# Kernel tuning notes

Measured on AMD Instinct MI355X. Metric: run time of the kernel, lower is better.

Reference implementation:

```python
import jax, jax.numpy as jnp
import numpy as np

B, L, D = 2, 2048, 2048
H, KVH, HD, FD = 8, 1, 256, 64   # heads, kv heads, head_dim, feature_dim
CHUNK = 64


def setup_inputs() -> dict:
    key = jax.random.key(0)
    ks = jax.random.split(key, 8)
    hidden_states = jax.random.normal(ks[0], (B, L, D), dtype=jnp.float32)
    # Gemma-style RoPE tables over half the head dim
    half = HD // 2
    inv_freq = 1.0 / (10000.0 ** (jnp.arange(half, dtype=jnp.float32) / half))
    ang = jnp.arange(L, dtype=jnp.float32)[:, None] * inv_freq[None, :]  # [L, half]
    freqs_cos, freqs_sin = jnp.cos(ang), jnp.sin(ang)
    mask = jnp.ones((1, 1, L, L), dtype=bool)  # unused in linear path
    s = 0.02
    Wq = jax.random.normal(ks[1], (D, H * HD), dtype=jnp.float32) * s
    Wk = jax.random.normal(ks[2], (D, KVH * HD), dtype=jnp.float32) * s
    Wv = jax.random.normal(ks[3], (D, KVH * HD), dtype=jnp.float32) * s
    Wo = jax.random.normal(ks[4], (H * HD, D), dtype=jnp.float32) * s
    fmq = jax.random.normal(ks[5], (H, HD, FD), dtype=jnp.float32) * s
    fmk = jax.random.normal(ks[6], (H, HD, FD), dtype=jnp.float32) * s
    return dict(hidden_states=hidden_states, freqs_cos=freqs_cos, freqs_sin=freqs_sin,
                mask=mask, Wq=Wq, Wk=Wk, Wv=Wv, Wo=Wo, fmq=fmq, fmk=fmk)


def _rope(x, cos, sin):
    # x: [B, L, h, HD]; Gemma complex RoPE: first half = real, second half = imag
    half = x.shape[-1] // 2
    x1, x2 = x[..., :half], x[..., half:]
    c = cos[None, :, None, :]
    s = sin[None, :, None, :]
    return jnp.concatenate([x1 * c - x2 * s, x1 * s + x2 * c], axis=-1)


def _hedgehog(x, W):
    # x: [B, H, L, HD], W: [H, HD, FD] -> softmax over cat([xW, -xW]) -> [B,H,L,2*FD]
    p = jnp.einsum('bhld,hdf->bhlf', x, W)
    return jax.nn.softmax(jnp.concatenate([p, -p], axis=-1), axis=-1)


def _chunk_linear_attn(q, k, v, chunk=CHUNK):
    # q,k: [B,H,L,F]; v: [B,H,L,HD]; chunked causal linear attention
    b, h, l, f = q.shape
    dv = v.shape[-1]
    n = l // chunk
    q = q.reshape(b, h, n, chunk, f) * (f ** -0.5)
    k = k.reshape(b, h, n, chunk, f)
    v = v.reshape(b, h, n, chunk, dv)
    kv = jnp.einsum('bhncf,bhncd->bhnfd', k, v)            # per-chunk KV
    kv = jnp.cumsum(kv, axis=2)
    kv = jnp.concatenate([jnp.zeros_like(kv[:, :, :1]), kv[:, :, :-1]], axis=2)  # exclusive prefix
    inter = jnp.einsum('bhncf,bhnfd->bhncd', q, kv)        # cross-chunk term
    s = jnp.einsum('bhnif,bhnjf->bhnij', q, k)             # intra-chunk scores
    tri = jnp.tril(jnp.ones((chunk, chunk), dtype=bool))
    s = jnp.where(tri, s, 0.0)
    intra = jnp.einsum('bhnij,bhnjd->bhnid', s, v)
    return (inter + intra).reshape(b, h, l, dv)


def reference(hidden_states, freqs_cos, freqs_sin, mask, Wq, Wk, Wv, Wo, fmq, fmk):
    b, l, _ = hidden_states.shape
    q = (hidden_states @ Wq).reshape(b, l, H, HD)
    k = (hidden_states @ Wk).reshape(b, l, KVH, HD)
    v = (hidden_states @ Wv).reshape(b, l, KVH, HD)
    q = _rope(q, freqs_cos, freqs_sin)
    k = _rope(k, freqs_cos, freqs_sin)
    # repeat_interleave kv heads to num_heads (MQA expansion)
    rep = H // KVH
    k = jnp.repeat(k, rep, axis=2)
    v = jnp.repeat(v, rep, axis=2)
    q = jnp.transpose(q, (0, 2, 1, 3))  # [B,H,L,HD]
    k = jnp.transpose(k, (0, 2, 1, 3))
    v = jnp.transpose(v, (0, 2, 1, 3))
    q = _hedgehog(q, fmq)
    k = _hedgehog(k, fmk)
    o = _chunk_linear_attn(q, k, v)                         # [B,H,L,HD]
    o = jnp.transpose(o, (0, 2, 1, 3)).reshape(b, l, H * HD)
    return o @ Wo
```

## Files before the change

kernel.cpp:

```cpp
#include <hip/hip_runtime.h>

#define B_ 2
#define L_ 2048
#define D_ 2048
#define H_ 8
#define HD_ 256
#define FD_ 64
#define F_ 128
#define NC_ 32
#define M_ (B_*L_)
#define SCALE_Q 0.08838834764831845f

typedef unsigned short u16;
typedef __attribute__((ext_vector_type(8))) short bf16x8;
typedef __attribute__((ext_vector_type(8))) unsigned short u16x8;
typedef __attribute__((ext_vector_type(16))) float f32x16;
typedef __attribute__((ext_vector_type(4))) unsigned int u32x4;

#define FMA4(a_, s_, v_) { (a_).x += (s_)*(v_).x; (a_).y += (s_)*(v_).y; \
                           (a_).z += (s_)*(v_).z; (a_).w += (s_)*(v_).w; }


__device__ __forceinline__ u16 bf16_rne(float x) {
  unsigned u = __float_as_uint(x);
  return (u16)((u + 0x7fffu + ((u >> 16) & 1u)) >> 16);
}
__device__ __forceinline__ void bf16_split(float x, u16& h, u16& l) {
  unsigned u = __float_as_uint(x);
  unsigned hb = (u + 0x7fffu + ((u >> 16) & 1u)) >> 16;
  h = (u16)hb;
  float hf = __uint_as_float(hb << 16);
  l = bf16_rne(x - hf);
}

__device__ __forceinline__ void gl_lds16(const u16* g, u16* l) {
  __builtin_amdgcn_global_load_lds(
      (const __attribute__((address_space(1))) unsigned int*)g,
      (__attribute__((address_space(3))) unsigned int*)l, 16, 0, 0);
}

__device__ __forceinline__ size_t kvb_off(int d, int f) {
  return (size_t)(((d >> 7) & 1) * 16384 + ((f >> 5) & 3) * 4096 +
                  ((d >> 6) & 1) * 2048 + ((f >> 4) & 1) * 1024 +
                  ((d >> 5) & 1) * 512 + ((f >> 3) & 1) * 256 +
                  (d & 31) * 8 + (f & 7));
}

__device__ __forceinline__ void wtrans_body(const float* __restrict__ W, int Nsrc,
                                            int n0, u16* __restrict__ dst,
                                            int P, int kt) {
  int t = threadIdx.x;
  int nn = t & 127, kh = t >> 7;
  const float* src = W + (size_t)(kt * 32 + kh * 16) * Nsrc + n0 + nn;
  u16x8 u0, u1;
  #pragma unroll
  for (int kk = 0; kk < 8; ++kk) u0[kk] = bf16_rne(src[(size_t)kk * Nsrc]);
  #pragma unroll
  for (int kk = 0; kk < 8; ++kk) u1[kk] = bf16_rne(src[(size_t)(kk + 8) * Nsrc]);
  size_t base = ((size_t)P * 64 + kt) * 4096 + (size_t)((nn >> 6) & 1) * 2048
              + (size_t)kh * 1024 + (size_t)((nn >> 5) & 1) * 512
              + (size_t)(nn & 31) * 8;
  *(u16x8*)(dst + base) = u0;
  *(u16x8*)(dst + base + 256) = u1;
}

__global__ __launch_bounds__(256)
void prep_kernel(const float* __restrict__ hs,
                 const float* __restrict__ Wq, const float* __restrict__ Wk,
                 const float* __restrict__ Wv,
                 u16* __restrict__ hsHt, u16* __restrict__ hsLt,
                 u16* __restrict__ WTh) {
  int bid = blockIdx.x;
  if (bid < 4096) {
    int gid = bid * 256 + threadIdx.x;
    int r = gid >> 8, u = gid & 255;
    const float* src = hs + (size_t)r * 2048 + u * 8;
    float4 v0 = *(const float4*)src, v1 = *(const float4*)(src + 4);
    float vals[8] = {v0.x, v0.y, v0.z, v0.w, v1.x, v1.y, v1.z, v1.w};
    u16x8 hv, lv;
    #pragma unroll
    for (int j = 0; j < 8; ++j) { u16 hh, ll; bf16_split(vals[j], hh, ll); hv[j] = hh; lv[j] = ll; }
    size_t off = ((size_t)(r >> 6) * 64 + (u >> 2)) * 2048
               + (size_t)((u >> 1) & 1) * 1024 + (size_t)((r >> 5) & 1) * 512
               + (size_t)(u & 1) * 256 + (size_t)(r & 31) * 8;
    *(u16x8*)(hsHt + off) = hv;
    *(u16x8*)(hsLt + off) = lv;
  } else {
    int idx = bid - 4096;
    int P = idx >> 6, kt = idx & 63;
    const float* W; int Nsrc, n0;
    if (P < 16)      { W = Wq; Nsrc = 2048; n0 = P * 128; }
    else if (P < 18) { W = Wk; Nsrc = 256;  n0 = (P - 16) * 128; }
    else             { W = Wv; Nsrc = 256;  n0 = (P - 18) * 128; }
    wtrans_body(W, Nsrc, n0, WTh, P, kt);
  }
}

__global__ __launch_bounds__(256)
void prep_o(const float* __restrict__ o, u16* __restrict__ oHt,
            u16* __restrict__ oLt) {
  int gid = blockIdx.x * 256 + threadIdx.x;
  int r = gid >> 8, u = gid & 255;
  const float* src = o + (size_t)r * 2048 + u * 8;
  float4 v0 = *(const float4*)src, v1 = *(const float4*)(src + 4);
  float vals[8] = {v0.x, v0.y, v0.z, v0.w, v1.x, v1.y, v1.z, v1.w};
  u16x8 hv, lv;
  #pragma unroll
  for (int j = 0; j < 8; ++j) { u16 hh, ll; bf16_split(vals[j], hh, ll); hv[j] = hh; lv[j] = ll; }
  size_t off = ((size_t)(r >> 6) * 64 + (u >> 2)) * 2048
             + (size_t)((u >> 1) & 1) * 1024 + (size_t)((r >> 5) & 1) * 512
             + (size_t)(u & 1) * 256 + (size_t)(r & 31) * 8;
  *(u16x8*)(oHt + off) = hv;
  *(u16x8*)(oLt + off) = lv;
}

__global__ __launch_bounds__(256)
void wtrans_wo(const float* __restrict__ Wo, u16* __restrict__ WoTh) {
  wtrans_body(Wo, 2048, blockIdx.x * 128, WoTh, blockIdx.x, blockIdx.y);
}

__device__ __forceinline__ void mfma_body(
    const u16* __restrict__ AtH, const u16* __restrict__ AtL,
    const u16* __restrict__ Bt, float* __restrict__ C, int cstride,
    int bm, int bn) {
  __shared__ __align__(16) u16 AsH[2048];
  __shared__ __align__(16) u16 AsL[2048];
  __shared__ __align__(16) u16 Bs[4096];
  const int t = threadIdx.x, lane = t & 63, wv = t >> 6;
  const u16* aSrc = (wv ? AtL : AtH) + (size_t)bm * 131072 + lane * 8;
  const u16* bSrc = Bt + (size_t)bn * 262144 + wv * 2048 + lane * 8;
  u16* aDst = wv ? AsL : AsH;
  u16* bDst = Bs + wv * 2048;

  f32x16 acc[2][2];
  #pragma unroll
  for (int a = 0; a < 2; ++a)
    #pragma unroll
    for (int b2 = 0; b2 < 2; ++b2)
      #pragma unroll
      for (int r = 0; r < 16; ++r) acc[a][b2][r] = 0.f;

  for (int kt = 0; kt < 64; ++kt) {
    const u16* ak = aSrc + (size_t)kt * 2048;
    const u16* bk = bSrc + (size_t)kt * 4096;
    __syncthreads();
    #pragma unroll
    for (int c = 0; c < 4; ++c) {
      gl_lds16(ak + c * 512, aDst + c * 512);
      gl_lds16(bk + c * 512, bDst + c * 512);
    }
    __syncthreads();

    #pragma unroll
    for (int ks = 0; ks < 2; ++ks) {
      const u16* ph = AsH + ks * 1024 + lane * 8;
      const u16* pl = AsL + ks * 1024 + lane * 8;
      const u16* pb = Bs + wv * 2048 + ks * 1024 + lane * 8;
      bf16x8 a0 = *(const bf16x8*)ph;
      bf16x8 a1 = *(const bf16x8*)(ph + 512);
      bf16x8 b0 = *(const bf16x8*)pb;
      bf16x8 b1 = *(const bf16x8*)(pb + 512);
      acc[0][0] = __builtin_amdgcn_mfma_f32_32x32x16_bf16(a0, b0, acc[0][0], 0, 0, 0);
      acc[0][1] = __builtin_amdgcn_mfma_f32_32x32x16_bf16(a0, b1, acc[0][1], 0, 0, 0);
      acc[1][0] = __builtin_amdgcn_mfma_f32_32x32x16_bf16(a1, b0, acc[1][0], 0, 0, 0);
      acc[1][1] = __builtin_amdgcn_mfma_f32_32x32x16_bf16(a1, b1, acc[1][1], 0, 0, 0);
      bf16x8 l0 = *(const bf16x8*)pl;
      bf16x8 l1 = *(const bf16x8*)(pl + 512);
      acc[0][0] = __builtin_amdgcn_mfma_f32_32x32x16_bf16(l0, b0, acc[0][0], 0, 0, 0);
      acc[0][1] = __builtin_amdgcn_mfma_f32_32x32x16_bf16(l0, b1, acc[0][1], 0, 0, 0);
      acc[1][0] = __builtin_amdgcn_mfma_f32_32x32x16_bf16(l1, b0, acc[1][0], 0, 0, 0);
      acc[1][1] = __builtin_amdgcn_mfma_f32_32x32x16_bf16(l1, b1, acc[1][1], 0, 0, 0);
    }
  }

  const int fr = lane & 31, g = lane >> 5;
  float* Cp = C + (size_t)(bm * 64) * cstride + wv * 64;
  #pragma unroll
  for (int mt = 0; mt < 2; ++mt)
    #pragma unroll
    for (int nt = 0; nt < 2; ++nt) {
      #pragma unroll
      for (int r = 0; r < 16; ++r) {
        int row = mt * 32 + (r & 3) + 8 * (r >> 2) + 4 * g;
        Cp[(size_t)row * cstride + nt * 32 + fr] = acc[mt][nt][r];
      }
    }
}

#define SUB_ 20480

__device__ __forceinline__ void mfma_big_body(
    const u16* __restrict__ AtH, const u16* __restrict__ AtL,
    const u16* __restrict__ Bt, float* __restrict__ C, int cstride,
    int bm, int bn) {
  __shared__ __align__(16) u16 lds[3 * SUB_];
  const int t = threadIdx.x, lane = t & 63, wv = t >> 6;
  const int wm = wv >> 1, wn = wv & 1;

  const u16* gs[5];
  unsigned lo[5], gst[5];
  #pragma unroll
  for (int j = 0; j < 5; ++j) {
    int line = wv * 5 + j;
    if (line < 16) {
      gs[j] = AtH + ((size_t)(4 * bm + (line >> 2)) * 64) * 2048
                  + (size_t)(line & 3) * 512 + lane * 8;
      lo[j] = line * 512; gst[j] = 2048;
    } else if (line < 32) {
      int l2 = line - 16;
      gs[j] = AtL + ((size_t)(4 * bm + (l2 >> 2)) * 64) * 2048
                  + (size_t)(l2 & 3) * 512 + lane * 8;
      lo[j] = 8192 + l2 * 512; gst[j] = 2048;
    } else {
      int l3 = line - 32;
      gs[j] = Bt + (size_t)bn * 262144 + (size_t)l3 * 512 + lane * 8;
      lo[j] = 16384 + l3 * 512; gst[j] = 4096;
    }
  }

  f32x16 acc[2][2];
  #pragma unroll
  for (int a = 0; a < 2; ++a)
    #pragma unroll
    for (int b2 = 0; b2 < 2; ++b2)
      #pragma unroll
      for (int r = 0; r < 16; ++r) acc[a][b2][r] = 0.f;

  auto stage = [&](int kt_, int boff_) {
    #pragma unroll
    for (int j = 0; j < 5; ++j)
      gl_lds16(gs[j] + (size_t)kt_ * gst[j], lds + boff_ + lo[j]);
  };

  stage(0, 0);
  stage(1, SUB_);
  asm volatile("s_waitcnt vmcnt(5)" ::: "memory");
  __builtin_amdgcn_s_barrier();
  __builtin_amdgcn_sched_barrier(0);

  int cb = 0;
  for (int kt = 0; kt < 64; ++kt) {
    int sb = cb + 2 * SUB_; if (sb >= 3 * SUB_) sb -= 3 * SUB_;
    if (kt < 62) stage(kt + 2, sb);
    const u16* base = lds + cb;
    #pragma unroll
    for (int ks = 0; ks < 2; ++ks) {
      const u16* ph = base + wm * 2048 + ks * 1024 + lane * 8;
      const u16* pb = base + 16384 + wn * 2048 + ks * 1024 + lane * 8;
      bf16x8 a0 = *(const bf16x8*)ph;
      bf16x8 a1 = *(const bf16x8*)(ph + 512);
      bf16x8 l0 = *(const bf16x8*)(ph + 8192);
      bf16x8 l1 = *(const bf16x8*)(ph + 8704);
      bf16x8 b0 = *(const bf16x8*)pb;
      bf16x8 b1 = *(const bf16x8*)(pb + 512);
      __builtin_amdgcn_s_setprio(1);
      acc[0][0] = __builtin_amdgcn_mfma_f32_32x32x16_bf16(a0, b0, acc[0][0], 0, 0, 0);
      acc[0][1] = __builtin_amdgcn_mfma_f32_32x32x16_bf16(a0, b1, acc[0][1], 0, 0, 0);
      acc[1][0] = __builtin_amdgcn_mfma_f32_32x32x16_bf16(a1, b0, acc[1][0], 0, 0, 0);
      acc[1][1] = __builtin_amdgcn_mfma_f32_32x32x16_bf16(a1, b1, acc[1][1], 0, 0, 0);
      acc[0][0] = __builtin_amdgcn_mfma_f32_32x32x16_bf16(l0, b0, acc[0][0], 0, 0, 0);
      acc[0][1] = __builtin_amdgcn_mfma_f32_32x32x16_bf16(l0, b1, acc[0][1], 0, 0, 0);
      acc[1][0] = __builtin_amdgcn_mfma_f32_32x32x16_bf16(l1, b0, acc[1][0], 0, 0, 0);
      acc[1][1] = __builtin_amdgcn_mfma_f32_32x32x16_bf16(l1, b1, acc[1][1], 0, 0, 0);
      __builtin_amdgcn_s_setprio(0);
    }
    asm volatile("s_waitcnt lgkmcnt(0)" ::: "memory");
    if (kt < 62) asm volatile("s_waitcnt vmcnt(5)" ::: "memory");
    else         asm volatile("s_waitcnt vmcnt(0)" ::: "memory");
    __builtin_amdgcn_s_barrier();
    __builtin_amdgcn_sched_barrier(0);
    cb += SUB_; if (cb == 3 * SUB_) cb = 0;
  }

  const int fr = lane & 31, g = lane >> 5;
  float* Cp = C + (size_t)(bm * 256 + wm * 64) * cstride + wn * 64;
  #pragma unroll
  for (int mt = 0; mt < 2; ++mt)
    #pragma unroll
    for (int nt = 0; nt < 2; ++nt) {
      #pragma unroll
      for (int r = 0; r < 16; ++r) {
        int row = mt * 32 + (r & 3) + 8 * (r >> 2) + 4 * g;
        Cp[(size_t)row * cstride + nt * 32 + fr] = acc[mt][nt][r];
      }
    }
}

__global__ __launch_bounds__(512, 2)
void mfma_q(const u16* __restrict__ hsHt, const u16* __restrict__ hsLt,
            const u16* __restrict__ WTh, float* __restrict__ q) {
  mfma_big_body(hsHt, hsLt, WTh, q + blockIdx.x * 128, 2048,
                blockIdx.y, blockIdx.x);
}

__global__ __launch_bounds__(128, 4)
void mfma_kv(const u16* __restrict__ hsHt, const u16* __restrict__ hsLt,
             const u16* __restrict__ WTh,
             float* __restrict__ k, float* __restrict__ v) {
  int bn = blockIdx.x;
  float* Cb; int co;
  if (bn < 2) { Cb = k; co = bn * 128; }
  else        { Cb = v; co = (bn - 2) * 128; }
  mfma_body(hsHt, hsLt, WTh, Cb + co, 256, blockIdx.y, 16 + bn);
}

__global__ __launch_bounds__(512, 2)
void mfma_wo(const u16* __restrict__ oHt, const u16* __restrict__ oLt,
             const u16* __restrict__ WoTh, float* __restrict__ out) {
  mfma_big_body(oHt, oLt, WoTh, out + blockIdx.x * 128, 2048,
                blockIdx.y, blockIdx.x);
}

__device__ __forceinline__ float wave_max64(float v) {
  #pragma unroll
  for (int off = 32; off > 0; off >>= 1) v = fmaxf(v, __shfl_xor(v, off, 64));
  return v;
}
__device__ __forceinline__ float wave_sum64(float v) {
  #pragma unroll
  for (int off = 32; off > 0; off >>= 1) v += __shfl_xor(v, off, 64);
  return v;
}

__global__ __launch_bounds__(256)
void hedgehog_kernel(const float* __restrict__ q, const float* __restrict__ kx,
                     const float* __restrict__ fmq, const float* __restrict__ fmk,
                     const float* __restrict__ cosb, const float* __restrict__ sinb,
                     float* __restrict__ qf, float* __restrict__ kf) {
  __shared__ __align__(16) float rows[4][4][256];
  int bid = blockIdx.x;
  const float* x; const float* fm; float* out; int nh_in, gb;
  if (bid < 2048) { x = q;  fm = fmq; out = qf; nh_in = 8; gb = bid * 4; }
  else            { x = kx; fm = fmk; out = kf; nh_in = 1; gb = (bid - 2048) * 4; }
  int wave = threadIdx.x >> 6, lane = threadIdx.x & 63;
  int g = gb + wave;
  int l4 = g & (L_/4 - 1);
  int bh = g / (L_/4);
  int h = bh & 7, b = bh >> 3;
  int l0 = l4 * 4;
  size_t rstride = (nh_in == 1) ? (size_t)HD_ : (size_t)H_ * HD_;
  const float* xrow = (nh_in == 1)
      ? x + (size_t)(b * L_ + l0) * HD_
      : x + ((size_t)(b * L_ + l0) * H_ + h) * HD_;
  int dd = (lane & 31) * 4;
  #pragma unroll
  for (int r = 0; r < 4; ++r) {
    float4 v = *(const float4*)(xrow + r * rstride + lane * 4);
    float4 u;
    u.x = __shfl_xor(v.x, 32, 64); u.y = __shfl_xor(v.y, 32, 64);
    u.z = __shfl_xor(v.z, 32, 64); u.w = __shfl_xor(v.w, 32, 64);
    int l = l0 + r;
    float4 c = *(const float4*)(cosb + (size_t)l * 128 + dd);
    float4 s = *(const float4*)(sinb + (size_t)l * 128 + dd);
    float4 ro;
    if (lane < 32) {
      ro.x = v.x * c.x - u.x * s.x; ro.y = v.y * c.y - u.y * s.y;
      ro.z = v.z * c.z - u.z * s.z; ro.w = v.w * c.w - u.w * s.w;
    } else {
      ro.x = u.x * s.x + v.x * c.x; ro.y = u.y * s.y + v.y * c.y;
      ro.z = u.z * s.z + v.z * c.z; ro.w = u.w * s.w + v.w * c.w;
    }
    *(float4*)&rows[wave][r][lane * 4] = ro;
  }
  __syncthreads();

  const float* fmh = fm + (size_t)h * HD_ * FD_;
  float p0 = 0.f, p1 = 0.f, p2 = 0.f, p3 = 0.f;
  for (int d2 = 0; d2 < HD_; d2 += 4) {
    float w0 = fmh[(d2 + 0) * FD_ + lane];
    float w1 = fmh[(d2 + 1) * FD_ + lane];
    float w2 = fmh[(d2 + 2) * FD_ + lane];
    float w3 = fmh[(d2 + 3) * FD_ + lane];
    float4 r0 = *(const float4*)&rows[wave][0][d2];
    float4 r1 = *(const float4*)&rows[wave][1][d2];
    float4 r2 = *(const float4*)&rows[wave][2][d2];
    float4 r3 = *(const float4*)&rows[wave][3][d2];
    p0 += r0.x * w0 + r0.y * w1 + r0.z * w2 + r0.w * w3;
    p1 += r1.x * w0 + r1.y * w1 + r1.z * w2 + r1.w * w3;
    p2 += r2.x * w0 + r2.y * w1 + r2.z * w2 + r2.w * w3;
    p3 += r3.x * w0 + r3.y * w1 + r3.z * w2 + r3.w * w3;
  }
  float p[4] = {p0, p1, p2, p3};
  #pragma unroll
  for (int r = 0; r < 4; ++r) {
    float m = wave_max64(fabsf(p[r]));
    float e1 = __expf(p[r] - m);
    float e2 = __expf(-p[r] - m);
    float z = wave_sum64(e1 + e2);
    float inv = 1.0f / z;
    size_t base = ((size_t)bh * L_ + l0 + r) * F_;
    out[base + lane]      = e1 * inv;
    out[base + 64 + lane] = e2 * inv;
  }
}

__global__ __launch_bounds__(256)
void chunk_kv_kernel(const float* __restrict__ kf, const float* __restrict__ v,
                     u16* __restrict__ kvbH, u16* __restrict__ kvbL) {
  __shared__ __align__(16) float kfs[64][128];
  int n = blockIdx.x & (NC_ - 1), bh = blockIdx.x >> 5;
  int b = bh >> 3;
  const float* kfp = kf + ((size_t)bh * L_ + (size_t)n * 64) * F_;
  int t = threadIdx.x;
  #pragma unroll
  for (int it = 0; it < 8; ++it) {
    int flat = t * 4 + it * 1024;
    *(float4*)&kfs[flat >> 7][flat & 127] = *(const float4*)(kfp + flat);
  }
  __syncthreads();
  int dg = t & 63;
  int fg = t >> 6;
  const float* vp = v + (size_t)(b * L_ + n * 64) * HD_ + dg * 4;
  size_t cb = (size_t)blockIdx.x * 32768;
  #pragma unroll
  for (int pass = 0; pass < 4; ++pass) {
    int f0 = fg * 8 + pass * 32;
    float4 acc[8];
    #pragma unroll
    for (int i = 0; i < 8; ++i) acc[i] = make_float4(0.f, 0.f, 0.f, 0.f);
    for (int j = 0; j < 64; ++j) {
      float4 vv = *(const float4*)(vp + (size_t)j * HD_);
      float4 ka = *(const float4*)&kfs[j][f0];
      float4 kb = *(const float4*)&kfs[j][f0 + 4];
      FMA4(acc[0], ka.x, vv); FMA4(acc[1], ka.y, vv);
      FMA4(acc[2], ka.z, vv); FMA4(acc[3], ka.w, vv);
      FMA4(acc[4], kb.x, vv); FMA4(acc[5], kb.y, vv);
      FMA4(acc[6], kb.z, vv); FMA4(acc[7], kb.w, vv);
    }
    #pragma unroll
    for (int c = 0; c < 4; ++c) {
      u16x8 hv, lv;
      #pragma unroll
      for (int ff = 0; ff < 8; ++ff) {
        float xs = (c == 0) ? acc[ff].x : (c == 1) ? acc[ff].y
                 : (c == 2) ? acc[ff].z : acc[ff].w;
        u16 hh, ll; bf16_split(xs, hh, ll); hv[ff] = hh; lv[ff] = ll;
      }
      int d = dg * 4 + c;
      size_t off = cb + kvb_off(d, f0);
      *(u16x8*)(kvbH + off) = hv;
      *(u16x8*)(kvbL + off) = lv;
    }
  }
}

__global__ __launch_bounds__(256)
void chunk_scan_kernel(u16* __restrict__ kvbH, u16* __restrict__ kvbL) {
  int bh = blockIdx.x >> 4, g = blockIdx.x & 15;
  int d = threadIdx.x;
  size_t off = kvb_off(d, g * 8);
  float run[8] = {0.f, 0.f, 0.f, 0.f, 0.f, 0.f, 0.f, 0.f};
  for (int n = 0; n < NC_; ++n) {
    size_t a = ((size_t)(bh * 32 + n)) * 32768 + off;
    u16x8 hv = *(u16x8*)(kvbH + a);
    u16x8 lv = *(u16x8*)(kvbL + a);
    u16x8 oh, ol;
    #pragma unroll
    for (int c = 0; c < 8; ++c) {
      float val = __uint_as_float((unsigned)hv[c] << 16)
                + __uint_as_float((unsigned)lv[c] << 16);
      u16 hh, ll; bf16_split(run[c], hh, ll); oh[c] = hh; ol[c] = ll;
      run[c] += val;
    }
    *(u16x8*)(kvbH + a) = oh;
    *(u16x8*)(kvbL + a) = ol;
  }
}

#define MFB(a_, b_, c_) (c_) = __builtin_amdgcn_mfma_f32_32x32x16_bf16((a_), (b_), (c_), 0, 0, 0)

__global__ __launch_bounds__(256, 2)
void chunk_attn_kernel(const float* __restrict__ qf, const float* __restrict__ kf,
                       const float* __restrict__ v,
                       const u16* __restrict__ kvbH, const u16* __restrict__ kvbL,
                       float* __restrict__ o) {
  __shared__ __align__(16) u16 lds[32768];
  const int n = blockIdx.x & (NC_ - 1), bh = blockIdx.x >> 5;
  const int h = bh & 7, b = bh >> 3;
  const int t = threadIdx.x;
  const int w = t >> 6, i31 = t & 31, G = (t >> 5) & 1;
  const int l8 = (t & 63) * 8;

  {
    const float* qp = qf + ((size_t)bh * L_ + (size_t)n * 64) * F_;
    const float* kp = kf + ((size_t)bh * L_ + (size_t)n * 64) * F_;
    int o8 = t & 15, ib = t >> 4;
    #pragma unroll
    for (int iter = 0; iter < 4; ++iter) {
      int i = ib + iter * 16;
      int it = i >> 5, ks = o8 >> 1;
      int sub = (it * 8 + ks) * 512 + (o8 & 1) * 256 + (i & 31) * 8;
      {
        const float* src = qp + (size_t)i * 128 + o8 * 8;
        float4 a = *(const float4*)src, c = *(const float4*)(src + 4);
        float vals[8] = {a.x, a.y, a.z, a.w, c.x, c.y, c.z, c.w};
        u16x8 hv, lv;
        #pragma unroll
        for (int j = 0; j < 8; ++j) {
          u16 hh, ll; bf16_split(vals[j] * SCALE_Q, hh, ll);
          hv[j] = hh; lv[j] = ll;
        }
        *(u16x8*)(lds + sub) = hv;
        *(u16x8*)(lds + 8192 + sub) = lv;
      }
      {
        const float* src = kp + (size_t)i * 128 + o8 * 8;
        float4 a = *(const float4*)src, c = *(const float4*)(src + 4);
        float vals[8] = {a.x, a.y, a.z, a.w, c.x, c.y, c.z, c.w};
        u16x8 hv, lv;
        #pragma unroll
        for (int j = 0; j < 8; ++j) {
          u16 hh, ll; bf16_split(vals[j], hh, ll);
          hv[j] = hh; lv[j] = ll;
        }
        *(u16x8*)(lds + 16384 + sub) = hv;
        *(u16x8*)(lds + 24576 + sub) = lv;
      }
    }
  }
  __syncthreads();

  const u16* Lq  = lds;
  const u16* Lql = lds + 8192;
  const u16* Lk  = lds + 16384;
  const u16* Lkl = lds + 24576;

  f32x16 st[2][2];
  #pragma unroll
  for (int a = 0; a < 2; ++a)
    #pragma unroll
    for (int c = 0; c < 2; ++c)
      #pragma unroll
      for (int r = 0; r < 16; ++r) st[a][c][r] = 0.f;

  #pragma unroll
  for (int ks = 0; ks < 8; ++ks) {
    bf16x8 kh0 = *(const bf16x8*)(Lk  + ks * 512 + l8);
    bf16x8 kh1 = *(const bf16x8*)(Lk  + (8 + ks) * 512 + l8);
    bf16x8 kl0 = *(const bf16x8*)(Lkl + ks * 512 + l8);
    bf16x8 kl1 = *(const bf16x8*)(Lkl + (8 + ks) * 512 + l8);
    bf16x8 qh0 = *(const bf16x8*)(Lq  + ks * 512 + l8);
    bf16x8 qh1 = *(const bf16x8*)(Lq  + (8 + ks) * 512 + l8);
    bf16x8 ql0 = *(const bf16x8*)(Lql + ks * 512 + l8);
    bf16x8 ql1 = *(const bf16x8*)(Lql + (8 + ks) * 512 + l8);
    MFB(kh0, qh0, st[0][0]); MFB(kh0, ql0, st[0][0]); MFB(kl0, qh0, st[0][0]);
    MFB(kh0, qh1, st[0][1]); MFB(kh0, ql1, st[0][1]); MFB(kl0, qh1, st[0][1]);
    MFB(kh1, qh0, st[1][0]); MFB(kh1, ql0, st[1][0]); MFB(kl1, qh0, st[1][0]);
    MFB(kh1, qh1, st[1][1]); MFB(kh1, ql1, st[1][1]); MFB(kl1, qh1, st[1][1]);
  }

  bf16x8 sfH[2][4], sfL[2][4];
  #pragma unroll
  for (int mt = 0; mt < 2; ++mt) {
    int iv = mt * 32 + i31;
    #pragma unroll
    for (int ksj = 0; ksj < 4; ++ksj) {
      const int jt = ksj >> 1, kb = ksj & 1;
      unsigned ph[4], pl[4];
      #pragma unroll
      for (int half = 0; half < 2; ++half) {
        u16 hh[4], ll[4];
        #pragma unroll
        for (int c = 0; c < 4; ++c) {
          int r = 8 * kb + 4 * half + c;
          int jv = jt * 32 + (r & 3) + 8 * (r >> 2) + 4 * G;
          float mv = (jv <= iv) ? st[jt][mt][r] : 0.f;
          u16 h_, l_; bf16_split(mv, h_, l_);
          hh[c] = h_; ll[c] = l_;
        }
        ph[half * 2 + 0] = (unsigned)hh[0] | ((unsigned)hh[1] << 16);
        ph[half * 2 + 1] = (unsigned)hh[2] | ((unsigned)hh[3] << 16);
        pl[half * 2 + 0] = (unsigned)ll[0] | ((unsigned)ll[1] << 16);
        pl[half * 2 + 1] = (unsigned)ll[2] | ((unsigned)ll[3] << 16);
      }
      unsigned rH1 = (unsigned)__shfl_xor((int)(G ? ph[0] : ph[2]), 32, 64);
      unsigned rH2 = (unsigned)__shfl_xor((int)(G ? ph[1] : ph[3]), 32, 64);
      unsigned rL1 = (unsigned)__shfl_xor((int)(G ? pl[0] : pl[2]), 32, 64);
      unsigned rL2 = (unsigned)__shfl_xor((int)(G ? pl[1] : pl[3]), 32, 64);
      u32x4 wH, wL;
      wH[0] = G ? rH1 : ph[0]; wH[1] = G ? rH2 : ph[1];
      wH[2] = G ? ph[2] : rH1; wH[3] = G ? ph[3] : rH2;
      wL[0] = G ? rL1 : pl[0]; wL[1] = G ? rL2 : pl[1];
      wL[2] = G ? pl[2] : rL1; wL[3] = G ? pl[3] : rL2;
      sfH[mt][ksj] = __builtin_bit_cast(bf16x8, wH);
      sfL[mt][ksj] = __builtin_bit_cast(bf16x8, wL);
    }
  }

  f32x16 acc[2][2];
  #pragma unroll
  for (int a = 0; a < 2; ++a)
    #pragma unroll
    for (int c = 0; c < 2; ++c)
      #pragma unroll
      for (int r = 0; r < 16; ++r) acc[a][c][r] = 0.f;

  {
    const float* vp = v + (size_t)(b * L_ + n * 64) * HD_;
    #pragma unroll
    for (int nt = 0; nt < 2; ++nt) {
      #pragma unroll
      for (int ksj = 0; ksj < 4; ++ksj) {
        const float* vsrc = vp + (size_t)(ksj * 16 + G * 8) * HD_
                          + w * 64 + nt * 32 + i31;
        u16x8 vh, vl;
        #pragma unroll
        for (int c = 0; c < 8; ++c) {
          u16 hh, ll; bf16_split(vsrc[(size_t)c * HD_], hh, ll);
          vh[c] = hh; vl[c] = ll;
        }
        bf16x8 vH = __builtin_bit_cast(bf16x8, vh);
        bf16x8 vL = __builtin_bit_cast(bf16x8, vl);
        MFB(sfH[0][ksj], vH, acc[0][nt]); MFB(sfL[0][ksj], vH, acc[0][nt]);
        MFB(sfH[0][ksj], vL, acc[0][nt]);
        MFB(sfH[1][ksj], vH, acc[1][nt]); MFB(sfL[1][ksj], vH, acc[1][nt]);
        MFB(sfH[1][ksj], vL, acc[1][nt]);
      }
    }
  }

  {
    size_t cb = (size_t)blockIdx.x * 32768;
    #pragma unroll
    for (int ks = 0; ks < 8; ++ks) {
      bf16x8 qa_h0 = *(const bf16x8*)(Lq  + ks * 512 + l8);
      bf16x8 qa_h1 = *(const bf16x8*)(Lq  + (8 + ks) * 512 + l8);
      bf16x8 qa_l0 = *(const bf16x8*)(Lql + ks * 512 + l8);
      bf16x8 qa_l1 = *(const bf16x8*)(Lql + (8 + ks) * 512 + l8);
      #pragma unroll
      for (int nt = 0; nt < 2; ++nt) {
        size_t base = cb + kvb_off(w * 64 + nt * 32, ks * 16) + l8;
        bf16x8 kvH = *(const bf16x8*)((const short*)(kvbH + base));
        bf16x8 kvL = *(const bf16x8*)((const short*)(kvbL + base));
        MFB(qa_h0, kvH, acc[0][nt]); MFB(qa_l0, kvH, acc[0][nt]);
        MFB(qa_h0, kvL, acc[0][nt]);
        MFB(qa_h1, kvH, acc[1][nt]); MFB(qa_l1, kvH, acc[1][nt]);
        MFB(qa_h1, kvL, acc[1][nt]);
      }
    }
  }

  float* op = o + ((size_t)(b * L_ + n * 64)) * 2048 + h * 256 + w * 64;
  #pragma unroll
  for (int mt = 0; mt < 2; ++mt)
    #pragma unroll
    for (int nt = 0; nt < 2; ++nt)
      #pragma unroll
      for (int r = 0; r < 16; ++r) {
        int row = mt * 32 + (r & 3) + 8 * (r >> 2) + 4 * G;
        op[(size_t)row * 2048 + nt * 32 + i31] = acc[mt][nt][r];
      }
}

extern "C" void kernel_launch(void* const* d_in, const int* in_sizes, int n_in,
                              void* d_out, int out_size, void* d_ws, size_t ws_size,
                              hipStream_t stream) {
  const float* hs   = (const float*)d_in[0];
  const float* fcos = (const float*)d_in[1];
  const float* fsin = (const float*)d_in[2];
  const float* Wq  = (const float*)d_in[4];
  const float* Wk  = (const float*)d_in[5];
  const float* Wv  = (const float*)d_in[6];
  const float* Wo  = (const float*)d_in[7];
  const float* fmq = (const float*)d_in[8];
  const float* fmk = (const float*)d_in[9];
  float* out = (float*)d_out;

  float* ws = (float*)d_ws;
  float* q  = ws;
  float* k  = q  + (size_t)M_ * 2048;
  float* v  = k  + (size_t)M_ * 256;
  float* qf = v  + (size_t)M_ * 256;
  float* kf = qf + (size_t)B_ * H_ * L_ * F_;
  float* kvr = kf + (size_t)B_ * H_ * L_ * F_;

  u16* hsHt = (u16*)kvr;
  u16* hsLt = hsHt + (size_t)M_ * 2048;
  u16* WTh  = hsLt + (size_t)M_ * 2048;
  u16* kvbH = (u16*)kvr;
  u16* kvbL = kvbH + (size_t)512 * 32768;
  u16* WoTh = (u16*)kvr;
  float* o  = q;
  u16* oHt  = (u16*)qf;
  u16* oLt  = (u16*)kf;

  prep_kernel<<<4096 + 1280, 256, 0, stream>>>(hs, Wq, Wk, Wv, hsHt, hsLt, WTh);
  mfma_q<<<dim3(16, 16), 512, 0, stream>>>(hsHt, hsLt, WTh, q);
  mfma_kv<<<dim3(4, 64), 128, 0, stream>>>(hsHt, hsLt, WTh, k, v);
  hedgehog_kernel<<<2048 + 2048, 256, 0, stream>>>(q, k, fmq, fmk, fcos, fsin, qf, kf);
  chunk_kv_kernel<<<B_ * H_ * NC_, 256, 0, stream>>>(kf, v, kvbH, kvbL);
  chunk_scan_kernel<<<256, 256, 0, stream>>>(kvbH, kvbL);
  chunk_attn_kernel<<<B_ * H_ * NC_, 256, 0, stream>>>(qf, kf, v, kvbH, kvbL, o);
  prep_o<<<4096, 256, 0, stream>>>(o, oHt, oLt);
  wtrans_wo<<<dim3(16, 64), 256, 0, stream>>>(Wo, WoTh);
  mfma_wo<<<dim3(16, 16), 512, 0, stream>>>(oHt, oLt, WoTh, out);
}
```

Baseline: 558.4 us.

## Split GEMM k-step into two interleaved halves and pre-split V to bf16 once

The big MFMA GEMM main loop now issues its LDS fragment reads and async global-to-LDS loads in two half-steps, each fenced by barriers, so memory traffic interleaves with MFMA work at a finer grain. Separately, a new prep_v kernel converts V into hi/lo bf16 in an MFMA-friendly layout once per batch-chunk. The attention kernel then loads ready fragments instead of redoing the strided fp32 gathers and splits for every head. The cost is one more launch, extra buffers reusing the k workspace, and more barriers per GEMM iteration.

```diff
diff --git a/kernel.cpp b/kernel.cpp
--- a/kernel.cpp
+++ b/kernel.cpp
@@ -44,6 +44,12 @@
                   ((d >> 6) & 1) * 2048 + ((f >> 4) & 1) * 1024 +
                   ((d >> 5) & 1) * 512 + ((f >> 3) & 1) * 256 +
                   (d & 31) * 8 + (f & 7));
+}
+__device__ __forceinline__ size_t vb_off(int d, int j) {
+  return (size_t)(((d >> 7) & 1) * 8192 + ((j >> 5) & 1) * 4096 +
+                  ((d >> 6) & 1) * 2048 + ((j >> 4) & 1) * 1024 +
+                  ((d >> 5) & 1) * 512 + ((j >> 3) & 1) * 256 +
+                  (d & 31) * 8 + (j & 7));
 }
 
 __device__ __forceinline__ void wtrans_body(const float* __restrict__ W, int Nsrc,
@@ -112,6 +118,28 @@
              + (size_t)(u & 1) * 256 + (size_t)(r & 31) * 8;
   *(u16x8*)(oHt + off) = hv;
   *(u16x8*)(oLt + off) = lv;
+}
+
+__global__ __launch_bounds__(256)
+void prep_v(const float* __restrict__ v, u16* __restrict__ vbH,
+            u16* __restrict__ vbL) {
+  int bn = blockIdx.x;
+  const float* vp = v + (size_t)bn * 64 * HD_;
+  size_t cbout = (size_t)bn * 16384;
+  int d = threadIdx.x;
+  #pragma unroll
+  for (int it = 0; it < 8; ++it) {
+    int j0 = it * 8;
+    u16x8 hv, lv;
+    #pragma unroll
+    for (int c = 0; c < 8; ++c) {
+      u16 hh, ll; bf16_split(vp[(size_t)(j0 + c) * HD_ + d], hh, ll);
+      hv[c] = hh; lv[c] = ll;
+    }
+    size_t off = cbout + vb_off(d, j0);
+    *(u16x8*)(vbH + off) = hv;
+    *(u16x8*)(vbL + off) = lv;
+  }
 }
 
 __global__ __launch_bounds__(256)
@@ -188,6 +216,7 @@
 }
 
 #define SUB_ 20480
+#define MFB(a_, b_, c_) (c_) = __builtin_amdgcn_mfma_f32_32x32x16_bf16((a_), (b_), (c_), 0, 0, 0)
 
 __device__ __forceinline__ void mfma_big_body(
     const u16* __restrict__ AtH, const u16* __restrict__ AtL,
@@ -226,14 +255,10 @@
       #pragma unroll
       for (int r = 0; r < 16; ++r) acc[a][b2][r] = 0.f;
 
-  auto stage = [&](int kt_, int boff_) {
-    #pragma unroll
-    for (int j = 0; j < 5; ++j)
-      gl_lds16(gs[j] + (size_t)kt_ * gst[j], lds + boff_ + lo[j]);
-  };
-
-  stage(0, 0);
-  stage(1, SUB_);
+  #pragma unroll
+  for (int j = 0; j < 5; ++j) gl_lds16(gs[j], lds + lo[j]);
+  #pragma unroll
+  for (int j = 0; j < 5; ++j) gl_lds16(gs[j] + gst[j], lds + SUB_ + lo[j]);
   asm volatile("s_waitcnt vmcnt(5)" ::: "memory");
   __builtin_amdgcn_s_barrier();
   __builtin_amdgcn_sched_barrier(0);
@@ -241,30 +266,52 @@
   int cb = 0;
   for (int kt = 0; kt < 64; ++kt) {
     int sb = cb + 2 * SUB_; if (sb >= 3 * SUB_) sb -= 3 * SUB_;
-    if (kt < 62) stage(kt + 2, sb);
     const u16* base = lds + cb;
-    #pragma unroll
-    for (int ks = 0; ks < 2; ++ks) {
-      const u16* ph = base + wm * 2048 + ks * 1024 + lane * 8;
-      const u16* pb = base + 16384 + wn * 2048 + ks * 1024 + lane * 8;
-      bf16x8 a0 = *(const bf16x8*)ph;
-      bf16x8 a1 = *(const bf16x8*)(ph + 512);
-      bf16x8 l0 = *(const bf16x8*)(ph + 8192);
-      bf16x8 l1 = *(const bf16x8*)(ph + 8704);
-      bf16x8 b0 = *(const bf16x8*)pb;
-      bf16x8 b1 = *(const bf16x8*)(pb + 512);
-      __builtin_amdgcn_s_setprio(1);
-      acc[0][0] = __builtin_amdgcn_mfma_f32_32x32x16_bf16(a0, b0, acc[0][0], 0, 0, 0);
-      acc[0][1] = __builtin_amdgcn_mfma_f32_32x32x16_bf16(a0, b1, acc[0][1], 0, 0, 0);
-      acc[1][0] = __builtin_amdgcn_mfma_f32_32x32x16_bf16(a1, b0, acc[1][0], 0, 0, 0);
-      acc[1][1] = __builtin_amdgcn_mfma_f32_32x32x16_bf16(a1, b1, acc[1][1], 0, 0, 0);
-      acc[0][0] = __builtin_amdgcn_mfma_f32_32x32x16_bf16(l0, b0, acc[0][0], 0, 0, 0);
-      acc[0][1] = __builtin_amdgcn_mfma_f32_32x32x16_bf16(l0, b1, acc[0][1], 0, 0, 0);
-      acc[1][0] = __builtin_amdgcn_mfma_f32_32x32x16_bf16(l1, b0, acc[1][0], 0, 0, 0);
-      acc[1][1] = __builtin_amdgcn_mfma_f32_32x32x16_bf16(l1, b1, acc[1][1], 0, 0, 0);
-      __builtin_amdgcn_s_setprio(0);
-    }
+    const u16* ph0 = base + wm * 2048 + lane * 8;
+    const u16* pb0 = base + 16384 + wn * 2048 + lane * 8;
+
+    bf16x8 a0 = *(const bf16x8*)(ph0);
+    bf16x8 a1 = *(const bf16x8*)(ph0 + 512);
+    bf16x8 l0 = *(const bf16x8*)(ph0 + 8192);
+    bf16x8 l1 = *(const bf16x8*)(ph0 + 8704);
+    bf16x8 b0 = *(const bf16x8*)(pb0);
+    bf16x8 b1 = *(const bf16x8*)(pb0 + 512);
+    if (kt < 62) {
+      gl_lds16(gs[0] + (size_t)(kt + 2) * gst[0], lds + sb + lo[0]);
+      gl_lds16(gs[1] + (size_t)(kt + 2) * gst[1], lds + sb + lo[1]);
+      gl_lds16(gs[2] + (size_t)(kt + 2) * gst[2], lds + sb + lo[2]);
+    }
+    __builtin_amdgcn_s_barrier();
     asm volatile("s_waitcnt lgkmcnt(0)" ::: "memory");
+    __builtin_amdgcn_sched_barrier(0);
+    __builtin_amdgcn_s_setprio(1);
+    MFB(a0, b0, acc[0][0]); MFB(a0, b1, acc[0][1]);
+    MFB(a1, b0, acc[1][0]); MFB(a1, b1, acc[1][1]);
+    MFB(l0, b0, acc[0][0]); MFB(l0, b1, acc[0][1]);
+    MFB(l1, b0, acc[1][0]); MFB(l1, b1, acc[1][1]);
+    __builtin_amdgcn_s_setprio(0);
+    __builtin_amdgcn_s_barrier();
+    __builtin_amdgcn_sched_barrier(0);
+
+    bf16x8 c0 = *(const bf16x8*)(ph0 + 1024);
+    bf16x8 c1 = *(const bf16x8*)(ph0 + 1536);
+    bf16x8 m0 = *(const bf16x8*)(ph0 + 9216);
+    bf16x8 m1 = *(const bf16x8*)(ph0 + 9728);
+    bf16x8 d0 = *(const bf16x8*)(pb0 + 1024);
+    bf16x8 d1 = *(const bf16x8*)(pb0 + 1536);
+    if (kt < 62) {
+      gl_lds16(gs[3] + (size_t)(kt + 2) * gst[3], lds + sb + lo[3]);
+      gl_lds16(gs[4] + (size_t)(kt + 2) * gst[4], lds + sb + lo[4]);
+    }
+    __builtin_amdgcn_s_barrier();
+    asm volatile("s_waitcnt lgkmcnt(0)" ::: "memory");
+    __builtin_amdgcn_sched_barrier(0);
+    __builtin_amdgcn_s_setprio(1);
+    MFB(c0, d0, acc[0][0]); MFB(c0, d1, acc[0][1]);
+    MFB(c1, d0, acc[1][0]); MFB(c1, d1, acc[1][1]);
+    MFB(m0, d0, acc[0][0]); MFB(m0, d1, acc[0][1]);
+    MFB(m1, d0, acc[1][0]); MFB(m1, d1, acc[1][1]);
+    __builtin_amdgcn_s_setprio(0);
     if (kt < 62) asm volatile("s_waitcnt vmcnt(5)" ::: "memory");
     else         asm volatile("s_waitcnt vmcnt(0)" ::: "memory");
     __builtin_amdgcn_s_barrier();
@@ -467,11 +514,9 @@
   }
 }
 
-#define MFB(a_, b_, c_) (c_) = __builtin_amdgcn_mfma_f32_32x32x16_bf16((a_), (b_), (c_), 0, 0, 0)
-
 __global__ __launch_bounds__(256, 2)
 void chunk_attn_kernel(const float* __restrict__ qf, const float* __restrict__ kf,
-                       const float* __restrict__ v,
+                       const u16* __restrict__ vbH, const u16* __restrict__ vbL,
                        const u16* __restrict__ kvbH, const u16* __restrict__ kvbL,
                        float* __restrict__ o) {
   __shared__ __align__(16) u16 lds[32768];
@@ -596,21 +641,14 @@
       for (int r = 0; r < 16; ++r) acc[a][c][r] = 0.f;
 
   {
-    const float* vp = v + (size_t)(b * L_ + n * 64) * HD_;
+    size_t vcb = ((size_t)(b * NC_ + n)) * 16384;
     #pragma unroll
     for (int nt = 0; nt < 2; ++nt) {
       #pragma unroll
       for (int ksj = 0; ksj < 4; ++ksj) {
-        const float* vsrc = vp + (size_t)(ksj * 16 + G * 8) * HD_
-                          + w * 64 + nt * 32 + i31;
-        u16x8 vh, vl;
-        #pragma unroll
-        for (int c = 0; c < 8; ++c) {
-          u16 hh, ll; bf16_split(vsrc[(size_t)c * HD_], hh, ll);
-          vh[c] = hh; vl[c] = ll;
-        }
-        bf16x8 vH = __builtin_bit_cast(bf16x8, vh);
-        bf16x8 vL = __builtin_bit_cast(bf16x8, vl);
+        size_t basev = vcb + vb_off(w * 64 + nt * 32, ksj * 16) + l8;
+        bf16x8 vH = *(const bf16x8*)((const short*)(vbH + basev));
+        bf16x8 vL = *(const bf16x8*)((const short*)(vbL + basev));
         MFB(sfH[0][ksj], vH, acc[0][nt]); MFB(sfL[0][ksj], vH, acc[0][nt]);
         MFB(sfH[0][ksj], vL, acc[0][nt]);
         MFB(sfH[1][ksj], vH, acc[1][nt]); MFB(sfL[1][ksj], vH, acc[1][nt]);
@@ -680,6 +718,8 @@
   u16* kvbH = (u16*)kvr;
   u16* kvbL = kvbH + (size_t)512 * 32768;
   u16* WoTh = (u16*)kvr;
+  u16* vbH  = (u16*)k;
+  u16* vbL  = vbH + (size_t)64 * 16384;
   float* o  = q;
   u16* oHt  = (u16*)qf;
   u16* oLt  = (u16*)kf;
@@ -688,9 +728,10 @@
   mfma_q<<<dim3(16, 16), 512, 0, stream>>>(hsHt, hsLt, WTh, q);
   mfma_kv<<<dim3(4, 64), 128, 0, stream>>>(hsHt, hsLt, WTh, k, v);
   hedgehog_kernel<<<2048 + 2048, 256, 0, stream>>>(q, k, fmq, fmk, fcos, fsin, qf, kf);
+  prep_v<<<B_ * NC_, 256, 0, stream>>>(v, vbH, vbL);
   chunk_kv_kernel<<<B_ * H_ * NC_, 256, 0, stream>>>(kf, v, kvbH, kvbL);
   chunk_scan_kernel<<<256, 256, 0, stream>>>(kvbH, kvbL);
-  chunk_attn_kernel<<<B_ * H_ * NC_, 256, 0, stream>>>(qf, kf, v, kvbH, kvbL, o);
+  chunk_attn_kernel<<<B_ * H_ * NC_, 256, 0, stream>>>(qf, kf, vbH, vbL, kvbH, kvbL, o);
   prep_o<<<4096, 256, 0, stream>>>(o, oHt, oLt);
   wtrans_wo<<<dim3(16, 64), 256, 0, stream>>>(Wo, WoTh);
   mfma_wo<<<dim3(16, 16), 512, 0, stream>>>(oHt, oLt, WoTh, out);
```

Result: faster. 537.9 us (-3.7%).
